# Kernel tuning notes

Measured on AMD Instinct MI355X. Metric: run time of the kernel, lower is better.

Reference implementation:

```python
import jax, jax.numpy as jnp
import numpy as np

B, S, D, H = 4, 1024, 1024, 16
HD = D // H
EPS = 1e-5


def layer_norm(x, scale, shift):
    mean = jnp.mean(x, axis=-1, keepdims=True)
    var = jnp.mean((x - mean) ** 2, axis=-1, keepdims=True)
    return scale * (x - mean) / jnp.sqrt(var + EPS) + shift


def gelu_tanh(x):
    c = jnp.sqrt(jnp.asarray(2.0 / jnp.pi, dtype=x.dtype))
    return 0.5 * x * (1.0 + jnp.tanh(c * (x + 0.044715 * x ** 3)))


def setup_inputs() -> dict:
    key = jax.random.key(0)
    ks = jax.random.split(key, 12)
    s = 0.02
    return {
        "x": jax.random.normal(ks[0], (B, S, D), dtype=jnp.float32),
        "attention_mask": jnp.ones((B, S), dtype=jnp.int32),
        "wq": jax.random.normal(ks[1], (D, D), dtype=jnp.float32) * s,
        "wk": jax.random.normal(ks[2], (D, D), dtype=jnp.float32) * s,
        "wv": jax.random.normal(ks[3], (D, D), dtype=jnp.float32) * s,
        "wo": jax.random.normal(ks[4], (D, D), dtype=jnp.float32) * s,
        "bo": jnp.zeros((D,), dtype=jnp.float32),
        "ln1_scale": jnp.ones((D,), dtype=jnp.float32),
        "ln1_shift": jnp.zeros((D,), dtype=jnp.float32),
        "ln2_scale": jnp.ones((D,), dtype=jnp.float32),
        "ln2_shift": jnp.zeros((D,), dtype=jnp.float32),
        "w1": jax.random.normal(ks[5], (D, 4 * D), dtype=jnp.float32) * s,
        "b1": jnp.zeros((4 * D,), dtype=jnp.float32),
        "w2": jax.random.normal(ks[6], (4 * D, D), dtype=jnp.float32) * s,
        "b2": jnp.zeros((D,), dtype=jnp.float32),
    }


def reference(x, attention_mask, wq, wk, wv, wo, bo, ln1_scale, ln1_shift,
              ln2_scale, ln2_shift, w1, b1, w2, b2):
    b, s, d = x.shape
    # --- pre-norm attention ---
    shortcut = x
    h = layer_norm(x, ln1_scale, ln1_shift)
    q = (h @ wq).reshape(b, s, H, HD).transpose(0, 2, 1, 3)  # bhsd
    k = (h @ wk).reshape(b, s, H, HD).transpose(0, 2, 1, 3)
    v = (h @ wv).reshape(b, s, H, HD).transpose(0, 2, 1, 3)
    scores = jnp.einsum('bhqd,bhkd->bhqk', q, k)
    causal = jnp.triu(jnp.ones((s, s), dtype=bool), k=1)  # True above diag -> masked
    neg_inf = jnp.asarray(-jnp.inf, dtype=scores.dtype)
    scores = jnp.where(causal, neg_inf, scores)
    pad = attention_mask[:, None, None, :].astype(bool)  # (b,1,1,k)
    scores = jnp.where(pad, scores, neg_inf)
    attn = jax.nn.softmax(scores / jnp.sqrt(jnp.asarray(HD, dtype=scores.dtype)), axis=-1)
    ctx = jnp.einsum('bhqk,bhkd->bhqd', attn, v)
    ctx = ctx.transpose(0, 2, 1, 3).reshape(b, s, d)
    x = shortcut + (ctx @ wo + bo)
    # --- pre-norm FFN ---
    shortcut = x
    h = layer_norm(x, ln2_scale, ln2_shift)
    h = gelu_tanh(h @ w1 + b1) @ w2 + b2
    return shortcut + h
```

## Files before the change

kernel.cpp:

```cpp
#include <hip/hip_runtime.h>
#include <hip/hip_bf16.h>
#include <math.h>

#define B_ 4
#define S_ 1024
#define D_ 1024
#define H_ 16
#define HD_ 64

typedef __hip_bfloat16 bf16_t;
typedef __attribute__((ext_vector_type(8))) short bf16x8;
typedef __attribute__((ext_vector_type(4))) float floatx4;

__device__ __forceinline__ float bf2f(ushort u) {
  return __uint_as_float((unsigned)u << 16);
}

__global__ __launch_bounds__(256) void prep_kernel(
    const float* __restrict__ x, const float* __restrict__ ln1s,
    const float* __restrict__ ln1b, bf16_t* __restrict__ h,
    const float* __restrict__ wq, const float* __restrict__ wk,
    const float* __restrict__ wv, const float* __restrict__ wo,
    const float* __restrict__ w1, const float* __restrict__ w2,
    bf16_t* __restrict__ wqkv_t, bf16_t* __restrict__ wo_t,
    bf16_t* __restrict__ w1_t, bf16_t* __restrict__ w2_t) {
  const int id = blockIdx.x;
  if (id < 4096) {
    const int row = id;
    float4 v = ((const float4*)(x + (size_t)row * D_))[threadIdx.x];
    float s = v.x + v.y + v.z + v.w;
    float ss = v.x * v.x + v.y * v.y + v.z * v.z + v.w * v.w;
#pragma unroll
    for (int off = 32; off > 0; off >>= 1) {
      s += __shfl_xor(s, off);
      ss += __shfl_xor(ss, off);
    }
    __shared__ float ls[4], lss[4], stats[2];
    const int wave = threadIdx.x >> 6, lane = threadIdx.x & 63;
    if (lane == 0) { ls[wave] = s; lss[wave] = ss; }
    __syncthreads();
    if (threadIdx.x == 0) {
      float t = ls[0] + ls[1] + ls[2] + ls[3];
      float tt = lss[0] + lss[1] + lss[2] + lss[3];
      float mean = t * (1.0f / D_);
      stats[0] = mean;
      stats[1] = rsqrtf(tt * (1.0f / D_) - mean * mean + 1e-5f);
    }
    __syncthreads();
    const float mean = stats[0], rstd = stats[1];
    float4 sc = ((const float4*)ln1s)[threadIdx.x];
    float4 sh = ((const float4*)ln1b)[threadIdx.x];
    bf16_t ob[4];
    ob[0] = __float2bfloat16(sc.x * (v.x - mean) * rstd + sh.x);
    ob[1] = __float2bfloat16(sc.y * (v.y - mean) * rstd + sh.y);
    ob[2] = __float2bfloat16(sc.z * (v.z - mean) * rstd + sh.z);
    ob[3] = __float2bfloat16(sc.w * (v.w - mean) * rstd + sh.w);
    *(ushort4*)(h + (size_t)row * D_ + threadIdx.x * 4) = *(ushort4*)ob;
    return;
  }
  const float* W;
  bf16_t* Wt;
  int K, N, n0, k0;
  if (id < 8192) {
    const int t = id - 4096, which = t >> 10, tile = t & 1023;
    n0 = (tile & 31) * 32;
    k0 = (tile >> 5) * 32;
    K = 1024; N = 1024;
    W = which == 0 ? wq : which == 1 ? wk : which == 2 ? wv : wo;
    Wt = which < 3 ? wqkv_t + (size_t)which * 1024 * 1024 : wo_t;
  } else if (id < 12288) {
    const int tile = id - 8192;
    n0 = (tile & 127) * 32;
    k0 = (tile >> 7) * 32;
    K = 1024; N = 4096;
    W = w1; Wt = w1_t;
  } else {
    const int tile = id - 12288;
    n0 = (tile & 31) * 32;
    k0 = (tile >> 5) * 32;
    K = 4096; N = 1024;
    W = w2; Wt = w2_t;
  }
  __shared__ float t[32][33];
  const int lx = threadIdx.x & 31, ly = threadIdx.x >> 5;
#pragma unroll
  for (int r = ly; r < 32; r += 8) t[r][lx] = W[(size_t)(k0 + r) * N + n0 + lx];
  __syncthreads();
#pragma unroll
  for (int r = ly; r < 32; r += 8)
    Wt[(size_t)(n0 + r) * K + k0 + lx] = __float2bfloat16(t[lx][r]);
}

__global__ __launch_bounds__(256) void mgemm_kernel(const bf16_t* __restrict__ A,
                                                    const bf16_t* __restrict__ Bt,
                                                    const float* __restrict__ bias,
                                                    void* __restrict__ C,
                                                    int M, int N, int K, int Kc,
                                                    int Mt, int Nt, int PM,
                                                    int mode) {
  __shared__ bf16_t As[128 * 64];
  __shared__ bf16_t Bs[128 * 64];
  const int tid = threadIdx.x;
  const int lane = tid & 63, w = tid >> 6;

  const int flat = blockIdx.x;
  const int xcd = flat & 7;
  int t0 = flat >> 3;
  const int mb = xcd % PM, nb = xcd / PM;
  const int mt = mb * Mt + (t0 % Mt);
  t0 /= Mt;
  const int nt = nb * Nt + (t0 % Nt);
  const int z = t0 / Nt;
  const int m0 = mt * 128, n0 = nt * 128;
  const int kz0 = z * Kc;
  const int wm = (w >> 1) * 64, wn = (w & 1) * 64;

  floatx4 zero = {0.f, 0.f, 0.f, 0.f};
  floatx4 acc[4][4];
#pragma unroll
  for (int i = 0; i < 4; i++)
#pragma unroll
    for (int j = 0; j < 4; j++) acc[i][j] = zero;

  const int ro8 = lane >> 3;
  const int g8 = ((lane & 7) ^ ro8) * 8;
  const bf16_t* ga[4];
  const bf16_t* gb[4];
  bf16_t* la[4];
  bf16_t* lb[4];
#pragma unroll
  for (int t = 0; t < 4; t++) {
    const int c = w + 4 * t;
    ga[t] = A + (size_t)(m0 + c * 8 + ro8) * K + g8;
    gb[t] = Bt + (size_t)(n0 + c * 8 + ro8) * K + g8;
    la[t] = &As[c * 512];
    lb[t] = &Bs[c * 512];
  }

  const int fr = lane & 15, quad = lane >> 4;

  for (int k0 = kz0; k0 < kz0 + Kc; k0 += 64) {
    __syncthreads();
#pragma unroll
    for (int t = 0; t < 4; t++) {
      __builtin_amdgcn_global_load_lds(
          (const __attribute__((address_space(1))) void*)(ga[t] + k0),
          (__attribute__((address_space(3))) void*)la[t], 16, 0, 0);
      __builtin_amdgcn_global_load_lds(
          (const __attribute__((address_space(1))) void*)(gb[t] + k0),
          (__attribute__((address_space(3))) void*)lb[t], 16, 0, 0);
    }
    __syncthreads();

#pragma unroll
    for (int ks = 0; ks < 2; ks++) {
      const int sq = ((quad + 4 * ks) ^ (fr & 7)) * 8;
      bf16x8 af[4], bfr[4];
#pragma unroll
      for (int i = 0; i < 4; i++) {
        af[i] = *(const bf16x8*)&As[(wm + i * 16 + fr) * 64 + sq];
        bfr[i] = *(const bf16x8*)&Bs[(wn + i * 16 + fr) * 64 + sq];
      }
#pragma unroll
      for (int i = 0; i < 4; i++)
#pragma unroll
        for (int j = 0; j < 4; j++)
          acc[i][j] = __builtin_amdgcn_mfma_f32_16x16x32_bf16(af[i], bfr[j],
                                                              acc[i][j], 0, 0, 0);
    }
  }

  bf16_t* Pz = (mode == 4) ? ((bf16_t*)C + (size_t)z * M * N) : nullptr;
#pragma unroll
  for (int j = 0; j < 4; j++) {
    const int col = n0 + wn + j * 16 + fr;
    const float bj = bias ? bias[col] : 0.f;
#pragma unroll
    for (int i = 0; i < 4; i++) {
      const int rbase = m0 + wm + i * 16 + quad * 4;
#pragma unroll
      for (int r = 0; r < 4; r++) {
        const int row = rbase + r;
        float c = acc[i][j][r] + bj;
        if (mode == 1) {
          const float xg = c;
          const float t = 0.7978845608028654f * (xg + 0.044715f * xg * xg * xg);
          const float th = 2.0f / (1.0f + __expf(-2.0f * t)) - 1.0f;
          c = 0.5f * xg * (1.0f + th);
        }
        if (mode == 4) {
          Pz[(size_t)row * N + col] = __float2bfloat16(c);
        } else {
          ((bf16_t*)C)[(size_t)row * N + col] = __float2bfloat16(c);
        }
      }
    }
  }
}

__global__ __launch_bounds__(256) void reduce2_ln_kernel(
    const bf16_t* __restrict__ P, size_t slice, const float* __restrict__ x,
    const float* __restrict__ bias, const float* __restrict__ scale,
    const float* __restrict__ shift, float* __restrict__ out,
    bf16_t* __restrict__ h) {
  const int row = blockIdx.x;
  const size_t e = (size_t)row * D_ + threadIdx.x * 4;
  const float4 xv = *(const float4*)(x + e);
  const ushort4 p0 = *(const ushort4*)((const ushort*)P + e);
  const ushort4 p1 = *(const ushort4*)((const ushort*)P + slice + e);
  const float4 bb = *(const float4*)(bias + threadIdx.x * 4);
  float4 v;
  v.x = xv.x + bf2f(p0.x) + bf2f(p1.x) + bb.x;
  v.y = xv.y + bf2f(p0.y) + bf2f(p1.y) + bb.y;
  v.z = xv.z + bf2f(p0.z) + bf2f(p1.z) + bb.z;
  v.w = xv.w + bf2f(p0.w) + bf2f(p1.w) + bb.w;
  *(float4*)(out + e) = v;

  float s = v.x + v.y + v.z + v.w;
  float ss = v.x * v.x + v.y * v.y + v.z * v.z + v.w * v.w;
#pragma unroll
  for (int off = 32; off > 0; off >>= 1) {
    s += __shfl_xor(s, off);
    ss += __shfl_xor(ss, off);
  }
  __shared__ float ls[4], lss[4], stats[2];
  const int wave = threadIdx.x >> 6, lane = threadIdx.x & 63;
  if (lane == 0) { ls[wave] = s; lss[wave] = ss; }
  __syncthreads();
  if (threadIdx.x == 0) {
    float t = ls[0] + ls[1] + ls[2] + ls[3];
    float tt = lss[0] + lss[1] + lss[2] + lss[3];
    float mean = t * (1.0f / D_);
    stats[0] = mean;
    stats[1] = rsqrtf(tt * (1.0f / D_) - mean * mean + 1e-5f);
  }
  __syncthreads();
  const float mean = stats[0], rstd = stats[1];
  const float4 sc = *(const float4*)(scale + threadIdx.x * 4);
  const float4 sh = *(const float4*)(shift + threadIdx.x * 4);
  bf16_t ob[4];
  ob[0] = __float2bfloat16(sc.x * (v.x - mean) * rstd + sh.x);
  ob[1] = __float2bfloat16(sc.y * (v.y - mean) * rstd + sh.y);
  ob[2] = __float2bfloat16(sc.z * (v.z - mean) * rstd + sh.z);
  ob[3] = __float2bfloat16(sc.w * (v.w - mean) * rstd + sh.w);
  *(ushort4*)(h + e) = *(ushort4*)ob;
}

__global__ __launch_bounds__(256) void reduce4_kernel(const bf16_t* __restrict__ P,
                                                      size_t slice,
                                                      const float* __restrict__ bias,
                                                      float* __restrict__ out,
                                                      int N) {
  const size_t e = ((size_t)blockIdx.x * 256 + threadIdx.x) * 4;
  const ushort* Pu = (const ushort*)P;
  const ushort4 p0 = *(const ushort4*)(Pu + e);
  const ushort4 p1 = *(const ushort4*)(Pu + slice + e);
  const ushort4 p2 = *(const ushort4*)(Pu + 2 * slice + e);
  const ushort4 p3 = *(const ushort4*)(Pu + 3 * slice + e);
  const float4 r = *(const float4*)(out + e);
  const float4 bb = *(const float4*)(bias + (int)(e % N));
  float4 o;
  o.x = r.x + bb.x + bf2f(p0.x) + bf2f(p1.x) + bf2f(p2.x) + bf2f(p3.x);
  o.y = r.y + bb.y + bf2f(p0.y) + bf2f(p1.y) + bf2f(p2.y) + bf2f(p3.y);
  o.z = r.z + bb.z + bf2f(p0.z) + bf2f(p1.z) + bf2f(p2.z) + bf2f(p3.z);
  o.w = r.w + bb.w + bf2f(p0.w) + bf2f(p1.w) + bf2f(p2.w) + bf2f(p3.w);
  *(float4*)(out + e) = o;
}

__global__ __launch_bounds__(256) void fattn_kernel(const bf16_t* __restrict__ QKV,
                                                    const int* __restrict__ mask,
                                                    bf16_t* __restrict__ O) {
  const int qt = gridDim.x - 1 - blockIdx.x;
  const int h = blockIdx.y, b = blockIdx.z;
  const int tid = threadIdx.x;
  const int lane = tid & 63, w = tid >> 6;
  const int tx = lane & 15, quad = lane >> 4;
  const int q0 = qt * 64;

  __shared__ ushort Ks[64 * 72];
  __shared__ ushort Vt[64 * 72];
  __shared__ ushort Ps[64 * 72];

  const ushort* qkv = (const ushort*)QKV;
  const size_t rowb = (size_t)b * S_ * 3072;
  const int koff = D_ + h * HD_, voff = 2 * D_ + h * HD_;

  bf16x8 qf[2];
#pragma unroll
  for (int ks = 0; ks < 2; ks++)
    qf[ks] = *(const bf16x8*)(qkv + rowb +
        (size_t)(q0 + w * 16 + tx) * 3072 + h * HD_ + ks * 32 + quad * 8);

  const short oneb = 0x3F80;
  bf16x8 vones = {oneb, oneb, oneb, oneb, oneb, oneb, oneb, oneb};

  floatx4 ctx[4], lacc;
#pragma unroll
  for (int nt = 0; nt < 4; nt++) {
    ctx[nt].x = 0.f; ctx[nt].y = 0.f; ctx[nt].z = 0.f; ctx[nt].w = 0.f;
  }
  lacc.x = 0.f; lacc.y = 0.f; lacc.z = 0.f; lacc.w = 0.f;

  for (int kt = 0; kt <= qt; kt++) {
    const int k0 = kt * 64;
    __syncthreads();
#pragma unroll
    for (int i = 0; i < 2; i++) {
      const int e = tid + i * 256;
      const int r = e >> 3, ch = (e & 7) * 8;
      *(uint4*)&Ks[r * 72 + ch] =
          *(const uint4*)(qkv + rowb + (size_t)(k0 + r) * 3072 + koff + ch);
    }
#pragma unroll
    for (int i = 0; i < 2; i++) {
      const int r = tid & 63;
      const int c8 = (tid >> 6) * 8 + i * 32;
      uint4 u = *(const uint4*)(qkv + rowb + (size_t)(k0 + r) * 3072 + voff + c8);
      const ushort* sv = (const ushort*)&u;
#pragma unroll
      for (int j = 0; j < 8; j++) Vt[(c8 + j) * 72 + r] = sv[j];
    }
    __syncthreads();

    floatx4 accS[4];
#pragma unroll
    for (int nt = 0; nt < 4; nt++) {
      accS[nt].x = 0.f; accS[nt].y = 0.f; accS[nt].z = 0.f; accS[nt].w = 0.f;
    }
#pragma unroll
    for (int ks = 0; ks < 2; ks++) {
      bf16x8 kf[4];
#pragma unroll
      for (int nt = 0; nt < 4; nt++)
        kf[nt] = *(const bf16x8*)&Ks[(nt * 16 + tx) * 72 + ks * 32 + quad * 8];
#pragma unroll
      for (int nt = 0; nt < 4; nt++)
        accS[nt] = __builtin_amdgcn_mfma_f32_16x16x32_bf16(qf[ks], kf[nt],
                                                           accS[nt], 0, 0, 0);
    }

#pragma unroll
    for (int nt = 0; nt < 4; nt++) {
      const int jc = k0 + nt * 16 + tx;
      const bool ok = mask[b * S_ + jc] != 0;
#pragma unroll
      for (int r = 0; r < 4; r++) {
        const int qrow = q0 + w * 16 + quad * 4 + r;
        float p = exp2f(accS[nt][r] * 0.1803368801111244f);
        if (jc > qrow || !ok) p = 0.f;
        Ps[(w * 16 + quad * 4 + r) * 72 + nt * 16 + tx] =
            ((__hip_bfloat16_raw)__float2bfloat16(p)).x;
      }
    }

#pragma unroll
    for (int ks = 0; ks < 2; ks++) {
      const bf16x8 pf = *(const bf16x8*)&Ps[(w * 16 + tx) * 72 + ks * 32 + quad * 8];
      bf16x8 vf[4];
#pragma unroll
      for (int nt = 0; nt < 4; nt++)
        vf[nt] = *(const bf16x8*)&Vt[(nt * 16 + tx) * 72 + ks * 32 + quad * 8];
#pragma unroll
      for (int nt = 0; nt < 4; nt++)
        ctx[nt] = __builtin_amdgcn_mfma_f32_16x16x32_bf16(pf, vf[nt],
                                                          ctx[nt], 0, 0, 0);
      lacc = __builtin_amdgcn_mfma_f32_16x16x32_bf16(pf, vones, lacc, 0, 0, 0);
    }
  }

  const size_t obase = (size_t)b * S_ * D_ + (size_t)h * HD_;
  float rinv[4];
#pragma unroll
  for (int r = 0; r < 4; r++) rinv[r] = 1.0f / lacc[r];
#pragma unroll
  for (int nt = 0; nt < 4; nt++)
#pragma unroll
    for (int r = 0; r < 4; r++) {
      const int q = q0 + w * 16 + quad * 4 + r;
      O[obase + (size_t)q * D_ + nt * 16 + tx] =
          __float2bfloat16(ctx[nt][r] * rinv[r]);
    }
}

extern "C" void kernel_launch(void* const* d_in, const int* in_sizes, int n_in,
                              void* d_out, int out_size, void* d_ws, size_t ws_size,
                              hipStream_t stream) {
  const float* x = (const float*)d_in[0];
  const int* mask = (const int*)d_in[1];
  const float* wq = (const float*)d_in[2];
  const float* wk = (const float*)d_in[3];
  const float* wv = (const float*)d_in[4];
  const float* wo = (const float*)d_in[5];
  const float* bo = (const float*)d_in[6];
  const float* ln2s = (const float*)d_in[9];
  const float* ln2b = (const float*)d_in[10];
  const float* w1 = (const float*)d_in[11];
  const float* b1 = (const float*)d_in[12];
  const float* w2 = (const float*)d_in[13];
  const float* b2 = (const float*)d_in[14];
  float* out = (float*)d_out;

  const int M = B_ * S_;
  char* ws = (char*)d_ws;
  const size_t MB = (size_t)1 << 20;
  bf16_t* qkv = (bf16_t*)(ws);
  bf16_t* ffn1 = (bf16_t*)(ws);
  bf16_t* ctx = (bf16_t*)(ws + 32 * MB);
  bf16_t* h = (bf16_t*)(ws + 40 * MB);
  bf16_t* wqkv_t = (bf16_t*)(ws + 48 * MB);
  bf16_t* wo_t = (bf16_t*)(ws + 54 * MB);
  bf16_t* w1_t = (bf16_t*)(ws + 56 * MB);
  bf16_t* w2_t = (bf16_t*)(ws + 64 * MB);
  bf16_t* Pa = (bf16_t*)(ws);
  bf16_t* Pf = (bf16_t*)(ws + 32 * MB);
  const size_t slice = (size_t)M * D_;

  prep_kernel<<<dim3(16384), 256, 0, stream>>>(x, (const float*)d_in[7],
                                               (const float*)d_in[8], h, wq, wk,
                                               wv, wo, w1, w2, wqkv_t, wo_t,
                                               w1_t, w2_t);

  mgemm_kernel<<<dim3(24 * 32), 256, 0, stream>>>(
      h, wqkv_t, nullptr, qkv, M, 3 * D_, D_, D_, 8, 12, 4, 0);

  fattn_kernel<<<dim3(S_ / 64, H_, B_), 256, 0, stream>>>(qkv, mask, ctx);

  mgemm_kernel<<<dim3(8 * 32 * 2), 256, 0, stream>>>(
      ctx, wo_t, nullptr, Pa, M, D_, D_, D_ / 2, 4, 8, 8, 4);

  reduce2_ln_kernel<<<dim3(M), 256, 0, stream>>>(Pa, slice, x, bo, ln2s, ln2b,
                                                 out, h);

  mgemm_kernel<<<dim3(32 * 32), 256, 0, stream>>>(
      h, w1_t, b1, ffn1, M, 4 * D_, D_, D_, 16, 8, 2, 1);

  mgemm_kernel<<<dim3(8 * 32 * 4), 256, 0, stream>>>(
      ffn1, w2_t, nullptr, Pf, M, D_, 4 * D_, D_, 8, 4, 4, 4);

  reduce4_kernel<<<dim3((size_t)M * D_ / 1024), 256, 0, stream>>>(
      Pf, slice, b2, out, D_);
}
```

Baseline: 377.3 us.

## Produce transposed V via separate GEMM and stream K/V to LDS with swizzle

The fused QKV projection is split into a QK GEMM and a second GEMM that writes V already transposed (D x M), so attention no longer transposes V element by element through shared memory. The attention kernel loads K and V tiles with global_load_lds direct-to-LDS copies into an XOR-swizzled, unpadded layout, and the P tile uses the same swizzle to avoid bank conflicts. This removes scalar LDS stores and the register staging of K/V loads, at the cost of an extra GEMM launch and a more intricate addressing scheme.

```diff
diff --git a/kernel.cpp b/kernel.cpp
--- a/kernel.cpp
+++ b/kernel.cpp
@@ -267,7 +267,8 @@
   *(float4*)(out + e) = o;
 }
 
-__global__ __launch_bounds__(256) void fattn_kernel(const bf16_t* __restrict__ QKV,
+__global__ __launch_bounds__(256) void fattn_kernel(const bf16_t* __restrict__ QK,
+                                                    const bf16_t* __restrict__ VT,
                                                     const int* __restrict__ mask,
                                                     bf16_t* __restrict__ O) {
   const int qt = gridDim.x - 1 - blockIdx.x;
@@ -277,19 +278,30 @@
   const int tx = lane & 15, quad = lane >> 4;
   const int q0 = qt * 64;
 
-  __shared__ ushort Ks[64 * 72];
-  __shared__ ushort Vt[64 * 72];
-  __shared__ ushort Ps[64 * 72];
-
-  const ushort* qkv = (const ushort*)QKV;
-  const size_t rowb = (size_t)b * S_ * 3072;
-  const int koff = D_ + h * HD_, voff = 2 * D_ + h * HD_;
+  __shared__ bf16_t Ks[64 * 64];
+  __shared__ bf16_t Vs[64 * 64];
+  __shared__ ushort Ps[64 * 64];
+
+  const int ro8 = lane >> 3;
+  const int g8 = ((lane & 7) ^ ro8) * 8;
+  const bf16_t* gk[2];
+  const bf16_t* gv[2];
+  bf16_t* lk[2];
+  bf16_t* lv[2];
+#pragma unroll
+  for (int t = 0; t < 2; t++) {
+    const int c = w + 4 * t;
+    gk[t] = QK + (size_t)((size_t)b * S_ + c * 8 + ro8) * 2048 + 1024 + h * HD_ + g8;
+    gv[t] = VT + (size_t)(h * HD_ + c * 8 + ro8) * 4096 + (size_t)b * S_ + g8;
+    lk[t] = &Ks[c * 512];
+    lv[t] = &Vs[c * 512];
+  }
 
   bf16x8 qf[2];
 #pragma unroll
   for (int ks = 0; ks < 2; ks++)
-    qf[ks] = *(const bf16x8*)(qkv + rowb +
-        (size_t)(q0 + w * 16 + tx) * 3072 + h * HD_ + ks * 32 + quad * 8);
+    qf[ks] = *(const bf16x8*)(QK + (size_t)((size_t)b * S_ + q0 + w * 16 + tx) * 2048 +
+                              h * HD_ + ks * 32 + quad * 8);
 
   const short oneb = 0x3F80;
   bf16x8 vones = {oneb, oneb, oneb, oneb, oneb, oneb, oneb, oneb};
@@ -305,20 +317,13 @@
     const int k0 = kt * 64;
     __syncthreads();
 #pragma unroll
-    for (int i = 0; i < 2; i++) {
-      const int e = tid + i * 256;
-      const int r = e >> 3, ch = (e & 7) * 8;
-      *(uint4*)&Ks[r * 72 + ch] =
-          *(const uint4*)(qkv + rowb + (size_t)(k0 + r) * 3072 + koff + ch);
-    }
-#pragma unroll
-    for (int i = 0; i < 2; i++) {
-      const int r = tid & 63;
-      const int c8 = (tid >> 6) * 8 + i * 32;
-      uint4 u = *(const uint4*)(qkv + rowb + (size_t)(k0 + r) * 3072 + voff + c8);
-      const ushort* sv = (const ushort*)&u;
-#pragma unroll
-      for (int j = 0; j < 8; j++) Vt[(c8 + j) * 72 + r] = sv[j];
+    for (int t = 0; t < 2; t++) {
+      __builtin_amdgcn_global_load_lds(
+          (const __attribute__((address_space(1))) void*)(gk[t] + (size_t)k0 * 2048),
+          (__attribute__((address_space(3))) void*)lk[t], 16, 0, 0);
+      __builtin_amdgcn_global_load_lds(
+          (const __attribute__((address_space(1))) void*)(gv[t] + k0),
+          (__attribute__((address_space(3))) void*)lv[t], 16, 0, 0);
     }
     __syncthreads();
 
@@ -329,10 +334,11 @@
     }
 #pragma unroll
     for (int ks = 0; ks < 2; ks++) {
+      const int sq = ((quad + 4 * ks) ^ (tx & 7)) * 8;
       bf16x8 kf[4];
 #pragma unroll
       for (int nt = 0; nt < 4; nt++)
-        kf[nt] = *(const bf16x8*)&Ks[(nt * 16 + tx) * 72 + ks * 32 + quad * 8];
+        kf[nt] = *(const bf16x8*)&Ks[(nt * 16 + tx) * 64 + sq];
 #pragma unroll
       for (int nt = 0; nt < 4; nt++)
         accS[nt] = __builtin_amdgcn_mfma_f32_16x16x32_bf16(qf[ks], kf[nt],
@@ -343,23 +349,27 @@
     for (int nt = 0; nt < 4; nt++) {
       const int jc = k0 + nt * 16 + tx;
       const bool ok = mask[b * S_ + jc] != 0;
+      const int col = nt * 16 + tx;
 #pragma unroll
       for (int r = 0; r < 4; r++) {
-        const int qrow = q0 + w * 16 + quad * 4 + r;
+        const int qq = quad * 4 + r;
+        const int qrow = q0 + w * 16 + qq;
         float p = exp2f(accS[nt][r] * 0.1803368801111244f);
         if (jc > qrow || !ok) p = 0.f;
-        Ps[(w * 16 + quad * 4 + r) * 72 + nt * 16 + tx] =
+        const int pc = ((((col >> 3) ^ (qq & 7)) << 3)) | (col & 7);
+        Ps[(w * 16 + qq) * 64 + pc] =
             ((__hip_bfloat16_raw)__float2bfloat16(p)).x;
       }
     }
 
 #pragma unroll
     for (int ks = 0; ks < 2; ks++) {
-      const bf16x8 pf = *(const bf16x8*)&Ps[(w * 16 + tx) * 72 + ks * 32 + quad * 8];
+      const int sq = ((quad + 4 * ks) ^ (tx & 7)) * 8;
+      const bf16x8 pf = *(const bf16x8*)&Ps[(w * 16 + tx) * 64 + sq];
       bf16x8 vf[4];
 #pragma unroll
       for (int nt = 0; nt < 4; nt++)
-        vf[nt] = *(const bf16x8*)&Vt[(nt * 16 + tx) * 72 + ks * 32 + quad * 8];
+        vf[nt] = *(const bf16x8*)&Vs[(nt * 16 + tx) * 64 + sq];
 #pragma unroll
       for (int nt = 0; nt < 4; nt++)
         ctx[nt] = __builtin_amdgcn_mfma_f32_16x16x32_bf16(pf, vf[nt],
@@ -403,7 +413,8 @@
   const int M = B_ * S_;
   char* ws = (char*)d_ws;
   const size_t MB = (size_t)1 << 20;
-  bf16_t* qkv = (bf16_t*)(ws);
+  bf16_t* qk = (bf16_t*)(ws);
+  bf16_t* vT = (bf16_t*)(ws + 16 * MB);
   bf16_t* ffn1 = (bf16_t*)(ws);
   bf16_t* ctx = (bf16_t*)(ws + 32 * MB);
   bf16_t* h = (bf16_t*)(ws + 40 * MB);
@@ -420,10 +431,14 @@
                                                wv, wo, w1, w2, wqkv_t, wo_t,
                                                w1_t, w2_t);
 
-  mgemm_kernel<<<dim3(24 * 32), 256, 0, stream>>>(
-      h, wqkv_t, nullptr, qkv, M, 3 * D_, D_, D_, 8, 12, 4, 0);
-
-  fattn_kernel<<<dim3(S_ / 64, H_, B_), 256, 0, stream>>>(qkv, mask, ctx);
+  mgemm_kernel<<<dim3(16 * 32), 256, 0, stream>>>(
+      h, wqkv_t, nullptr, qk, M, 2 * D_, D_, D_, 8, 8, 4, 0);
+
+  mgemm_kernel<<<dim3(8 * 32), 256, 0, stream>>>(
+      wqkv_t + (size_t)2 * 1024 * 1024, h, nullptr, vT, D_, M, D_, D_,
+      4, 8, 2, 0);
+
+  fattn_kernel<<<dim3(S_ / 64, H_, B_), 256, 0, stream>>>(qk, vT, mask, ctx);
 
   mgemm_kernel<<<dim3(8 * 32 * 2), 256, 0, stream>>>(
       ctx, wo_t, nullptr, Pa, M, D_, D_, D_ / 2, 4, 8, 8, 4);
```

After: 362.4 us. 3.9% less time.
